# Performance work log

Hardware: AMD Instinct MI355X
Metric: run time of the kernel (lower is better)

The kernel has to match this reference:

```python
import math
import jax, jax.numpy as jnp
import numpy as np

B, S, D = 2, 2048, 3584
H, KVH, HD = 28, 4, 128
ROPE_THETA = 1000000.0

def setup_inputs() -> dict:
    key = jax.random.key(0)
    k1, k2, k3, k4, k5 = jax.random.split(key, 5)
    s = 0.02
    return {
        'hidden_states': jax.random.normal(k1, (B, S, D), jnp.float32),
        'Wq': jax.random.normal(k2, (D, H * HD), jnp.float32) * s,
        'Wk': jax.random.normal(k3, (D, KVH * HD), jnp.float32) * s,
        'Wv': jax.random.normal(k4, (D, KVH * HD), jnp.float32) * s,
        'Wo': jax.random.normal(k5, (H * HD, D), jnp.float32) * s,
    }

def _rotate_half(x):
    x1, x2 = x[..., :x.shape[-1] // 2], x[..., x.shape[-1] // 2:]
    return jnp.concatenate((-x2, x1), axis=-1)

def _rope_tables(seq_len, dim, base):
    inv_freq = 1.0 / base ** (jnp.arange(0, dim, 2, dtype=jnp.float32) / dim)
    t = jnp.arange(seq_len, dtype=jnp.float32)
    freqs = jnp.outer(t, inv_freq)  # [S, dim/2]
    emb = jnp.concatenate((freqs, freqs), axis=-1)  # [S, dim]
    return jnp.cos(emb), jnp.sin(emb)

def reference(hidden_states, Wq, Wk, Wv, Wo):
    b, s, _ = hidden_states.shape
    q = (hidden_states @ Wq).reshape(b, s, H, HD)
    k = (hidden_states @ Wk).reshape(b, s, KVH, HD)
    v = (hidden_states @ Wv).reshape(b, s, KVH, HD)

    cos, sin = _rope_tables(s, HD, ROPE_THETA)
    cos = cos.astype(q.dtype)[None, :, None, :]  # [1,S,1,HD]
    sin = sin.astype(q.dtype)[None, :, None, :]
    q = q * cos + _rotate_half(q) * sin
    k = k * cos + _rotate_half(k) * sin

    groups = H // KVH  # 7
    k = jnp.repeat(k, groups, axis=2)
    v = jnp.repeat(v, groups, axis=2)

    q = jnp.transpose(q, (0, 2, 1, 3))  # [B,H,S,HD]
    k = jnp.transpose(k, (0, 2, 1, 3))
    v = jnp.transpose(v, (0, 2, 1, 3))

    scale = 1.0 / math.sqrt(HD)
    scores = jnp.einsum('bhqd,bhkd->bhqk', q, k) * scale
    causal = jnp.tril(jnp.ones((s, s), dtype=bool))[None, None]
    scores = scores + jnp.where(causal, 0.0, -1e9).astype(scores.dtype)
    attn = jax.nn.softmax(scores, axis=-1)
    out = jnp.einsum('bhqk,bhkd->bhqd', attn, v)
    out = jnp.transpose(out, (0, 2, 1, 3)).reshape(b, s, H * HD)
    return out @ Wo
```

## Files before the change

### kernel.cpp

```cpp
#include <hip/hip_runtime.h>
#include <hip/hip_bf16.h>
#include <cstdint>

typedef __attribute__((ext_vector_type(8))) __bf16 bf16x8;
typedef __attribute__((ext_vector_type(4))) float f32x4;
typedef unsigned short u16;

#define B_    2
#define S_    2048
#define D_    3584
#define H_    28
#define KVH_  4
#define HD_   128
#define GQA_  7
#define QKVN  4608
#define QK2SCALE 0.12751744416014806f

#define WAITV(N) asm volatile("s_waitcnt vmcnt(" #N ")" ::: "memory")
#define WAITL(N) asm volatile("s_waitcnt lgkmcnt(" #N ")" ::: "memory")

__device__ __forceinline__ u16 f2bf(float f){
  union { float f; uint32_t u; } v; v.f = f;
  uint32_t u = v.u + 0x7fffu + ((v.u >> 16) & 1u);
  return (u16)(u >> 16);
}
__device__ __forceinline__ float bf2f(u16 h){
  union { uint32_t u; float f; } v; v.u = ((uint32_t)h) << 16; return v.f;
}
__device__ __forceinline__ float exp2a(float x){
  float r; asm("v_exp_f32 %0, %1" : "=v"(r) : "v"(x)); return r;
}
__device__ __forceinline__ uint32_t cvtpk(float lo, float hi){
  uint32_t r; asm("v_cvt_pk_bf16_f32 %0, %1, %2" : "=v"(r) : "v"(lo), "v"(hi)); return r;
}

typedef void __attribute__((address_space(1))) as1void;
typedef void __attribute__((address_space(3))) as3void;
__device__ __forceinline__ void gload16(const void* g, void* l){
  __builtin_amdgcn_global_load_lds((as1void*)g, (as3void*)l, 16, 0, 0);
}

#define NB_CONVX 14336
#define NB_WQ    12544
#define NB_WK    1792
#define NB_WV    1792
#define NB_WO    12544
#define NB_TAB   512
__global__ __launch_bounds__(256) void prep_kernel(const float* __restrict__ X, u16* __restrict__ Xb,
                                                   const float* __restrict__ Wq, const float* __restrict__ Wk,
                                                   const float* __restrict__ Wv, const float* __restrict__ Wo,
                                                   u16* __restrict__ Wqkv, u16* __restrict__ Wot,
                                                   float* __restrict__ cost, float* __restrict__ sint){
  __shared__ float t[32][33];
  int id = blockIdx.x;
  if (id < NB_CONVX){
    int i = id*256 + threadIdx.x;
    float4 v = ((const float4*)X)[i];
    ushort4 o; o.x=f2bf(v.x); o.y=f2bf(v.y); o.z=f2bf(v.z); o.w=f2bf(v.w);
    ((ushort4*)Xb)[i] = o;
    return;
  }
  id -= NB_CONVX;
  if (id < NB_WQ + NB_WK + NB_WV + NB_WO){
    const float* src; u16* dst; int R, C;
    if (id < NB_WQ){ src = Wq; dst = Wqkv; R = D_; C = H_*HD_; }
    else if (id < NB_WQ + NB_WK){ id -= NB_WQ; src = Wk; dst = Wqkv + (size_t)(H_*HD_)*D_; R = D_; C = KVH_*HD_; }
    else if (id < NB_WQ + NB_WK + NB_WV){ id -= NB_WQ + NB_WK; src = Wv; dst = Wqkv + (size_t)(H_*HD_ + KVH_*HD_)*D_; R = D_; C = KVH_*HD_; }
    else { id -= NB_WQ + NB_WK + NB_WV; src = Wo; dst = Wot; R = H_*HD_; C = D_; }
    int nbx = C >> 5;
    int c0 = (id % nbx) << 5, r0 = (id / nbx) << 5;
    int r = threadIdx.x >> 5, c = threadIdx.x & 31;
    #pragma unroll
    for (int i=0;i<4;i++) t[r+8*i][c] = src[(size_t)(r0 + r + 8*i)*C + c0 + c];
    __syncthreads();
    #pragma unroll
    for (int i=0;i<4;i++) dst[(size_t)(c0 + r + 8*i)*R + r0 + c] = f2bf(t[c][r+8*i]);
    return;
  }
  id -= NB_WQ + NB_WK + NB_WV + NB_WO;
  int i = id*256 + threadIdx.x;
  int s = i >> 6, d = i & 63;
  float inv = powf(1.0e6f, -(float)d * (1.0f/64.0f));
  float a = (float)s * inv;
  cost[i] = cosf(a); sint[i] = sinf(a);
}

__global__ __launch_bounds__(256) void tbf16_kernel(const u16* __restrict__ in, u16* __restrict__ outp, int R, int C, int instride){
  const u16* inb = in + (size_t)blockIdx.z*R*instride;
  u16* outb = outp + (size_t)blockIdx.z*R*C;
  __shared__ u16 t[32][33];
  int r = threadIdx.x >> 5, c = threadIdx.x & 31;
  int r0 = blockIdx.y*32, c0 = blockIdx.x*32;
  #pragma unroll
  for (int i=0;i<4;i++) t[r+8*i][c] = inb[(size_t)(r0+r+8*i)*instride + c0+c];
  __syncthreads();
  #pragma unroll
  for (int i=0;i<4;i++) outb[(size_t)(c0+r+8*i)*R + r0+c] = t[c][r+8*i];
}

__global__ __launch_bounds__(256) void gemm128_kernel(const u16* __restrict__ A, const u16* __restrict__ Bt,
                                                      u16* __restrict__ C, int M, int N, int K, int ldc, int coloff,
                                                      const float* __restrict__ cost, const float* __restrict__ sint,
                                                      int ropeNmax){
  __shared__ u16 As[128*32];
  __shared__ u16 Bs[128*32];
  const int tid = threadIdx.x;
  const int l = tid & 63, lg = l >> 4, lm = l & 15;
  const int w = tid >> 6, wr = w >> 1, wc = w & 1;
  const int m0 = blockIdx.y * 128, n0 = blockIdx.x * 128;

  f32x4 acc[4][4];
  #pragma unroll
  for (int m=0;m<4;++m)
    #pragma unroll
    for (int n=0;n<4;++n) acc[m][n] = (f32x4){0.f,0.f,0.f,0.f};

  const int nkt = K >> 5;
  for (int kt = 0; kt < nkt; ++kt){
    __syncthreads();
    const int kb = kt*32;
    #pragma unroll
    for (int j = 0; j < 2; ++j){
      int g = j*256 + tid;
      int row = g >> 2, wi = g & 3;
      int ksrc = kb + ((wi ^ (row & 3)) << 3);
      gload16(A  + (size_t)(m0+row)*K + ksrc, (char*)As + j*4096 + (tid & 192)*16);
      gload16(Bt + (size_t)(n0+row)*K + ksrc, (char*)Bs + j*4096 + (tid & 192)*16);
    }
    __syncthreads();
    bf16x8 af[4], bfr[4];
    #pragma unroll
    for (int m = 0; m < 4; ++m){
      int r = wr*64 + m*16 + lm;
      af[m] = *(const bf16x8*)((const char*)As + r*64 + (lg ^ (r & 3))*16);
    }
    #pragma unroll
    for (int n = 0; n < 4; ++n){
      int r = (wc<<5) + ((n>>1)<<6) + ((n&1)<<4) + lm;
      bfr[n] = *(const bf16x8*)((const char*)Bs + r*64 + (lg ^ (r & 3))*16);
    }
    #pragma unroll
    for (int m = 0; m < 4; ++m)
      #pragma unroll
      for (int n = 0; n < 4; ++n)
        acc[m][n] = __builtin_amdgcn_mfma_f32_16x16x32_bf16(af[m], bfr[n], acc[m][n], 0,0,0);
  }

  if (n0 < ropeNmax){
    #pragma unroll
    for (int m=0;m<4;++m)
      #pragma unroll
      for (int n=0;n<2;++n)
        #pragma unroll
        for (int r=0;r<4;++r){
          int row = m0 + wr*64 + m*16 + lg*4 + r;
          int s = row & (S_-1);
          int d = (wc<<5) + (n<<4) + lm;
          float cv = cost[s*64+d], sv = sint[s*64+d];
          float lo = acc[m][n][r], hi = acc[m][n+2][r];
          acc[m][n][r]   = lo*cv - hi*sv;
          acc[m][n+2][r] = hi*cv + lo*sv;
        }
  }

  #pragma unroll
  for (int m=0;m<4;++m)
    #pragma unroll
    for (int n=0;n<4;++n)
      #pragma unroll
      for (int r=0;r<4;++r){
        int row = m0 + wr*64 + m*16 + lg*4 + r;
        int col = coloff + n0 + (wc<<5) + ((n>>1)<<6) + ((n&1)<<4) + lm;
        C[(size_t)row*ldc + col] = f2bf(acc[m][n][r]);
      }
}

template<bool OUTF32, bool ROPEQ>
__global__ __launch_bounds__(512) void gemm256_kernel(const u16* __restrict__ A, const u16* __restrict__ Bt,
                                                      void* __restrict__ Cv, int M, int N, int K, int nbx,
                                                      int ldc, int coloff,
                                                      const float* __restrict__ cost, const float* __restrict__ sint){
  extern __shared__ char lds[];
  const int tid = threadIdx.x;
  const int l = tid & 63, lg = l >> 4, lm = l & 15;
  const int w = tid >> 6, wr = w >> 2, wc = w & 3;
  const int srow = tid >> 3, swi = tid & 7;

  const int nwg = (int)gridDim.x;
  const int q8 = nwg >> 3, r8 = nwg & 7;
  const int xcd = blockIdx.x & 7, pos = blockIdx.x >> 3;
  const int wg = (xcd < r8 ? xcd*(q8+1) : r8*(q8+1) + (xcd - r8)*q8) + pos;
  const int m0 = (wg / nbx) * 256, n0 = (wg % nbx) * 256;

  f32x4 acc[8][4];
  #pragma unroll
  for (int m=0;m<8;++m)
    #pragma unroll
    for (int n=0;n<4;++n) acc[m][n] = (f32x4){0.f,0.f,0.f,0.f};
  bf16x8 aF[8][2], bF[4][2];

  auto stage = [&](int T, int ht){
    const u16* p = (ht < 2) ? (A + (size_t)(m0 + (ht << 7))*K)
                            : (Bt + (size_t)(n0 + ((ht - 2) << 7))*K);
    char* d = lds + ((size_t)(T & 1) << 16) + (ht << 14) + ((tid & 448) << 4);
    #pragma unroll
    for (int j = 0; j < 2; ++j){
      int r = (j << 6) + srow;
      gload16(p + (size_t)r*K + (size_t)T*64 + ((swi ^ (r & 7)) << 3), d + (j << 13));
    }
  };
  auto ldA = [&](int c, int mh){
    const char* base = lds + (c << 16) + (wr << 14);
    #pragma unroll
    for (int m = 0; m < 4; ++m){
      int r = ((mh*4 + m) << 4) + lm;
      #pragma unroll
      for (int kk = 0; kk < 2; ++kk)
        aF[mh*4+m][kk] = *(const bf16x8*)(base + r*128 + (((kk*4 + lg) ^ (r & 7)) << 4));
    }
  };
  auto ldB = [&](int c, int nh){
    #pragma unroll
    for (int n = 0; n < 2; ++n){
      int f = nh*2 + n;
      int rb = ((wc>>1)<<7) + ((wc&1)<<5) + ((f>>1)<<6) + ((f&1)<<4) + lm;
      const char* base = lds + (c << 16) + 32768 + ((rb >> 7) << 14);
      int ri = rb & 127;
      #pragma unroll
      for (int kk = 0; kk < 2; ++kk)
        bF[f][kk] = *(const bf16x8*)(base + ri*128 + (((kk*4 + lg) ^ (ri & 7)) << 4));
    }
  };
  auto mmaQ = [&](int mh, int nh){
    __builtin_amdgcn_s_setprio(1);
    #pragma unroll
    for (int m = 0; m < 4; ++m)
      #pragma unroll
      for (int n = 0; n < 2; ++n)
        #pragma unroll
        for (int kk = 0; kk < 2; ++kk)
          acc[mh*4+m][nh*2+n] = __builtin_amdgcn_mfma_f32_16x16x32_bf16(
              aF[mh*4+m][kk], bF[nh*2+n][kk], acc[mh*4+m][nh*2+n], 0,0,0);
    __builtin_amdgcn_s_setprio(0);
  };

  const int nkt = K >> 6;
  stage(0,0); stage(0,1); stage(0,2); stage(0,3);
  stage(1,2); stage(1,0); stage(1,1);
  WAITV(6);
  __builtin_amdgcn_s_barrier();

  for (int t = 0; t < nkt; ++t){
    const int c = t & 1;
    ldA(c,0); ldB(c,0); ldB(c,1);
    if (t + 1 < nkt) stage(t+1, 3);
    WAITL(4);
    __builtin_amdgcn_s_barrier();
    mmaQ(0,0);
    WAITL(0);
    __builtin_amdgcn_s_barrier();
    ldA(c,1);
    if (t + 2 < nkt) stage(t+2, 2);
    __builtin_amdgcn_s_barrier();
    mmaQ(0,1);
    WAITL(0);
    __builtin_amdgcn_s_barrier();
    if (t + 2 < nkt) stage(t+2, 0);
    __builtin_amdgcn_s_barrier();
    mmaQ(1,0);
    __builtin_amdgcn_s_barrier();
    if (t + 2 < nkt){ stage(t+2, 1); WAITV(6); }
    else if (t + 1 < nkt){ WAITV(0); }
    __builtin_amdgcn_s_barrier();
    mmaQ(1,1);
    __builtin_amdgcn_s_barrier();
  }

  if (ROPEQ){
    #pragma unroll
    for (int m=0;m<8;++m)
      #pragma unroll
      for (int n=0;n<2;++n)
        #pragma unroll
        for (int r=0;r<4;++r){
          int row = m0 + wr*128 + m*16 + lg*4 + r;
          int s = row & (S_-1);
          int d = ((wc&1)<<5) + (n<<4) + lm;
          float cv = cost[s*64+d], sv = sint[s*64+d];
          float lo = acc[m][n][r], hi = acc[m][n+2][r];
          acc[m][n][r]   = (lo*cv - hi*sv)*QK2SCALE;
          acc[m][n+2][r] = (hi*cv + lo*sv)*QK2SCALE;
        }
  }

  #pragma unroll
  for (int m = 0; m < 8; ++m)
    #pragma unroll
    for (int n = 0; n < 4; ++n)
      #pragma unroll
      for (int r = 0; r < 4; ++r){
        int row = m0 + wr*128 + m*16 + lg*4 + r;
        int col = coloff + n0 + ((wc>>1)<<7) + ((wc&1)<<5) + ((n>>1)<<6) + ((n&1)<<4) + lm;
        if (OUTF32) ((float*)Cv)[(size_t)row*ldc + col] = acc[m][n][r];
        else        ((u16*)Cv)[(size_t)row*ldc + col] = f2bf(acc[m][n][r]);
      }
}

__global__ __launch_bounds__(512, 4) void attn_kernel(const u16* __restrict__ QKV, const u16* __restrict__ Vt,
                                                      u16* __restrict__ O){
  __shared__ u16 Kl[2][8192];
  __shared__ u16 Vl[8192];
  const int id = blockIdx.x;
  const int qt = (S_/128 - 1) - id/(H_*B_);
  const int hb = id % (H_*B_);
  const int h = hb % H_, b = hb / H_;
  const int kvh = h / GQA_;
  const int tid = threadIdx.x;
  const int w = tid >> 6, l = tid & 63, lg = l >> 4, lm = l & 15;

  const int qrowA = qt*128 + w*16 + lm;
  const u16* qptr = QKV + (size_t)(b*S_ + qrowA)*QKVN + h*HD_;
  bf16x8 qf[4];
  #pragma unroll
  for (int ks = 0; ks < 4; ++ks) qf[ks] = *(const bf16x8*)(qptr + ks*32 + lg*8);
  WAITV(0);
  asm volatile("" :: "v"(qf[0]), "v"(qf[1]), "v"(qf[2]), "v"(qf[3]));

  const int qcol  = qrowA;
  const int qrowD = qt*128 + w*16 + lg*4;
  float m_run = -3.0e38f, l_run = 0.0f;
  f32x4 oacc[8];
  #pragma unroll
  for (int dn=0;dn<8;++dn) oacc[dn] = (f32x4){0.f,0.f,0.f,0.f};

  const u16* Kbase = QKV + (size_t)(b*S_)*QKVN + H_*HD_ + kvh*HD_;
  const u16* Vbase = Vt + (size_t)(b*KVH_ + kvh)*HD_*S_;

  auto stageK = [&](int bufi, int ktv){
    const int kb = ktv*64;
    #pragma unroll
    for (int j = 0; j < 2; ++j){
      int g = j*512 + tid;
      int kp = g >> 4, wik = g & 15;
      gload16(Kbase + (size_t)(kb + kp)*QKVN + (wik ^ (kp & 7))*8,
              (char*)Kl + bufi*16384 + j*8192 + (tid & 448)*16);
    }
  };
  auto stageV = [&](int ktv){
    const int kb = ktv*64;
    #pragma unroll
    for (int j = 0; j < 2; ++j){
      int g = j*512 + tid;
      int dd = g >> 3, wiv = g & 7;
      gload16(Vbase + (size_t)dd*S_ + kb + (wiv ^ (dd & 7))*8,
              (char*)Vl + j*8192 + (tid & 448)*16);
    }
  };

  const int nkt = 2*qt + 2;
  int cur = 0;
  stageK(0, 0); stageV(0); stageK(1, 1);

  auto iter = [&](int kt, bool domask){
    const bool last = (kt + 1 == nkt);
    if (last) WAITV(2); else WAITV(4);
    __builtin_amdgcn_s_barrier();
    const int cb = cur*16384;

    f32x4 sf[4];
    __builtin_amdgcn_s_setprio(1);
    #pragma unroll
    for (int n = 0; n < 4; ++n){
      sf[n] = (f32x4){0.f,0.f,0.f,0.f};
      int kp = n*16 + lm;
      #pragma unroll
      for (int ks = 0; ks < 4; ++ks){
        bf16x8 kf = *(const bf16x8*)((const char*)Kl + cb + kp*256 + (((ks*4 + lg) ^ (kp & 7))*16));
        sf[n] = __builtin_amdgcn_mfma_f32_16x16x32_bf16(kf, qf[ks], sf[n], 0,0,0);
      }
    }
    __builtin_amdgcn_s_setprio(0);

    float p[4][4];
    float rmax = -3.0e38f;
    #pragma unroll
    for (int n=0;n<4;++n)
      #pragma unroll
      for (int r=0;r<4;++r){
        float v = sf[n][r];
        if (domask && (kt*64 + n*16 + lg*4 + r) > qcol) v -= 1.0e9f;
        p[n][r] = v;
        rmax = fmaxf(rmax, v);
      }
    rmax = fmaxf(rmax, __shfl_xor(rmax, 16, 64));
    rmax = fmaxf(rmax, __shfl_xor(rmax, 32, 64));

    if (__any(rmax > m_run + 8.0f)){
      float mn = fmaxf(m_run, rmax);
      float corr = exp2a(m_run - mn);
      m_run = mn;
      l_run *= corr;
      float corr_r[4];
      #pragma unroll
      for (int r=0;r<4;++r) corr_r[r] = __shfl(corr, lg*4 + r, 64);
      #pragma unroll
      for (int dn=0;dn<8;++dn)
        #pragma unroll
        for (int r=0;r<4;++r) oacc[dn][r] *= corr_r[r];
    }
    float psum = 0.f;
    #pragma unroll
    for (int n=0;n<4;++n)
      #pragma unroll
      for (int r=0;r<4;++r){ p[n][r] = exp2a(p[n][r] - m_run); psum += p[n][r]; }
    l_run += psum;

    if (last) WAITV(0); else WAITV(2);
    __builtin_amdgcn_s_barrier();
    char* Pl = (char*)Kl + cb;
    {
      int q_ = w*16 + lm;
      #pragma unroll
      for (int n=0;n<4;++n)
        #pragma unroll
        for (int j=0;j<2;++j){
          uint32_t pk = cvtpk(p[n][2*j], p[n][2*j+1]);
          int kp = n*16 + lg*4 + 2*j;
          *(uint32_t*)(Pl + q_*128 + (((kp >> 3) ^ (q_ & 7))*16) + (kp & 7)*2) = pk;
        }
    }

    __builtin_amdgcn_s_setprio(1);
    #pragma unroll
    for (int ks=0; ks<2; ++ks){
      int q_ = w*16 + lm;
      bf16x8 pf = *(const bf16x8*)(Pl + q_*128 + (((ks*4 + lg) ^ (q_ & 7))*16));
      #pragma unroll
      for (int dn=0;dn<8;++dn){
        int dd = dn*16 + lm;
        bf16x8 vf = *(const bf16x8*)((const char*)Vl + dd*128 + (((ks*4 + lg) ^ (dd & 7))*16));
        oacc[dn] = __builtin_amdgcn_mfma_f32_16x16x32_bf16(pf, vf, oacc[dn], 0,0,0);
      }
    }
    __builtin_amdgcn_s_setprio(0);

    WAITL(0);
    __builtin_amdgcn_s_barrier();
    if (kt + 1 < nkt) stageV(kt+1);
    if (kt + 2 < nkt) stageK(cur, kt+2);
    cur ^= 1;
  };

  for (int kt = 0; kt < nkt - 2; ++kt) iter(kt, false);
  iter(nkt-2, true);
  iter(nkt-1, true);

  l_run += __shfl_xor(l_run, 16, 64);
  l_run += __shfl_xor(l_run, 32, 64);
  float inv = 1.0f / l_run;
  float inv_r[4];
  #pragma unroll
  for (int r=0;r<4;++r) inv_r[r] = __shfl(inv, lg*4 + r, 64);
  #pragma unroll
  for (int dn=0;dn<8;++dn)
    #pragma unroll
    for (int r=0;r<4;++r)
      O[(size_t)(b*S_ + qrowD + r)*(H_*HD_) + h*HD_ + dn*16 + lm] = f2bf(oacc[dn][r]*inv_r[r]);
}

extern "C" void kernel_launch(void* const* d_in, const int* in_sizes, int n_in,
                              void* d_out, int out_size, void* d_ws, size_t ws_size,
                              hipStream_t stream) {
  const float* X  = (const float*)d_in[0];
  const float* Wq = (const float*)d_in[1];
  const float* Wk = (const float*)d_in[2];
  const float* Wv = (const float*)d_in[3];
  const float* Wo = (const float*)d_in[4];
  float* out = (float*)d_out;

  char* ws = (char*)d_ws;
  size_t off = 0;
  auto alloc = [&](size_t bytes)->void*{ void* p = ws + off; off += (bytes + 255) & ~(size_t)255; return p; };
  const size_t MB = (size_t)B_*S_;
  u16* Xb   = (u16*)alloc(MB*D_*2);
  u16* Wqkv = (u16*)alloc((size_t)D_*QKVN*2);
  u16* Wot  = (u16*)alloc((size_t)H_*HD_*D_*2);
  u16* QKVb = (u16*)alloc(MB*QKVN*2);
  float* cost = (float*)alloc((size_t)S_*64*4);
  float* sint = (float*)alloc((size_t)S_*64*4);
  u16* AO  = Xb;
  u16* Vtg = Wqkv;

  (void)hipFuncSetAttribute(reinterpret_cast<const void*>(gemm256_kernel<false, true>),
                            hipFuncAttributeMaxDynamicSharedMemorySize, 131072);
  (void)hipFuncSetAttribute(reinterpret_cast<const void*>(gemm256_kernel<true, false>),
                            hipFuncAttributeMaxDynamicSharedMemorySize, 131072);

  prep_kernel<<<dim3(NB_CONVX + NB_WQ + NB_WK + NB_WV + NB_WO + NB_TAB), 256, 0, stream>>>(
      X, Xb, Wq, Wk, Wv, Wo, Wqkv, Wot, cost, sint);
  gemm256_kernel<false, true><<<dim3((D_/256)*(MB/256)), 512, 131072, stream>>>(
      Xb, Wqkv, QKVb, (int)MB, D_, D_, D_/256, QKVN, 0, cost, sint);
  gemm128_kernel<<<dim3((KVH_*HD_*2)/128, MB/128), 256, 0, stream>>>(
      Xb, Wqkv + (size_t)(H_*HD_)*D_, QKVb, (int)MB, KVH_*HD_*2, D_, QKVN, H_*HD_, cost, sint, KVH_*HD_);
  tbf16_kernel<<<dim3((KVH_*HD_)/32, S_/32, B_), 256, 0, stream>>>(QKVb + (H_+KVH_)*HD_, Vtg, S_, KVH_*HD_, QKVN);
  attn_kernel<<<dim3((S_/128)*H_*B_), 512, 0, stream>>>(QKVb, Vtg, AO);
  gemm256_kernel<true, false><<<dim3((D_/256)*(MB/256)), 512, 131072, stream>>>(
      AO, Wot, out, (int)MB, D_, H_*HD_, D_/256, D_, 0, cost, sint);
}
```

Before: 428.5 us.

## Double-buffer LDS tiles in GEMM kernel with prefetch two stages ahead

Replaces the single-buffered LDS tiles in the bf16 GEMM with a two-slot ring buffer. The next K-tile's global-to-LDS loads are issued while the current tile is consumed, synchronised with explicit vmcnt waits and raw barriers. MFMA sections also raise wave priority via s_setprio. The aim is to hide global load latency behind matrix math, at the cost of twice the LDS per block, which may lower occupancy.

```diff
diff --git a/kernel.cpp b/kernel.cpp
--- a/kernel.cpp
+++ b/kernel.cpp
@@ -102,8 +102,7 @@
                                                       u16* __restrict__ C, int M, int N, int K, int ldc, int coloff,
                                                       const float* __restrict__ cost, const float* __restrict__ sint,
                                                       int ropeNmax){
-  __shared__ u16 As[128*32];
-  __shared__ u16 Bs[128*32];
+  __shared__ char lds[32768];
   const int tid = threadIdx.x;
   const int l = tid & 63, lg = l >> 4, lm = l & 15;
   const int w = tid >> 6, wr = w >> 1, wc = w & 1;
@@ -115,35 +114,50 @@
     #pragma unroll
     for (int n=0;n<4;++n) acc[m][n] = (f32x4){0.f,0.f,0.f,0.f};
 
-  const int nkt = K >> 5;
-  for (int kt = 0; kt < nkt; ++kt){
-    __syncthreads();
-    const int kb = kt*32;
+  auto stage = [&](int T){
+    const int kb = T << 5;
+    char* base = lds + (size_t)(T & 1)*16384;
     #pragma unroll
     for (int j = 0; j < 2; ++j){
       int g = j*256 + tid;
       int row = g >> 2, wi = g & 3;
       int ksrc = kb + ((wi ^ (row & 3)) << 3);
-      gload16(A  + (size_t)(m0+row)*K + ksrc, (char*)As + j*4096 + (tid & 192)*16);
-      gload16(Bt + (size_t)(n0+row)*K + ksrc, (char*)Bs + j*4096 + (tid & 192)*16);
-    }
-    __syncthreads();
+      gload16(A  + (size_t)(m0+row)*K + ksrc, base + j*4096 + (tid & 192)*16);
+      gload16(Bt + (size_t)(n0+row)*K + ksrc, base + 8192 + j*4096 + (tid & 192)*16);
+    }
+  };
+
+  const int nkt = K >> 5;
+  stage(0); stage(1);
+  int cur = 0;
+  for (int t = 0; t < nkt; ++t){
+    if (t + 1 < nkt){ WAITV(4); }
+    else            { WAITV(0); }
+    __builtin_amdgcn_s_barrier();
+    const char* As = lds + (size_t)cur*16384;
+    const char* Bs = As + 8192;
     bf16x8 af[4], bfr[4];
     #pragma unroll
     for (int m = 0; m < 4; ++m){
       int r = wr*64 + m*16 + lm;
-      af[m] = *(const bf16x8*)((const char*)As + r*64 + (lg ^ (r & 3))*16);
+      af[m] = *(const bf16x8*)(As + r*64 + ((lg ^ (r & 3)) << 4));
     }
     #pragma unroll
     for (int n = 0; n < 4; ++n){
       int r = (wc<<5) + ((n>>1)<<6) + ((n&1)<<4) + lm;
-      bfr[n] = *(const bf16x8*)((const char*)Bs + r*64 + (lg ^ (r & 3))*16);
-    }
+      bfr[n] = *(const bf16x8*)(Bs + r*64 + ((lg ^ (r & 3)) << 4));
+    }
+    __builtin_amdgcn_s_setprio(1);
     #pragma unroll
     for (int m = 0; m < 4; ++m)
       #pragma unroll
       for (int n = 0; n < 4; ++n)
         acc[m][n] = __builtin_amdgcn_mfma_f32_16x16x32_bf16(af[m], bfr[n], acc[m][n], 0,0,0);
+    __builtin_amdgcn_s_setprio(0);
+    WAITL(0);
+    __builtin_amdgcn_s_barrier();
+    if (t + 2 < nkt) stage(t+2);
+    cur ^= 1;
   }
 
   if (n0 < ropeNmax){
```

After: 400.2 us, median of 2. 1.07x faster.
